# Performance work log

Measured on AMD Instinct MI355X. Metric: run time of the kernel, lower is better.

## Reference

```python
import jax, jax.numpy as jnp
import numpy as np

N = 100000
E = 3200000
H = 128
ED = 16
P = 6  # 2**(sample_hop+1)-2 with sample_hop=2


def setup_inputs() -> dict:
    key = jax.random.key(0)
    ks = jax.random.split(key, 8)
    q = jax.random.normal(ks[0], (N, H), jnp.float32)
    k = jax.random.normal(ks[1], (N, H), jnp.float32)
    v = jax.random.normal(ks[2], (N, H), jnp.float32)
    eigs = jax.random.normal(ks[3], (N, ED), jnp.float32)
    lambda0 = jnp.zeros((1,), jnp.float32)
    path_emb_w = jax.random.normal(ks[4], (P, 1), jnp.float32)
    indices = jax.random.randint(ks[5], (2, E), 0, N, dtype=jnp.int32)
    path_type = jax.random.randint(ks[6], (E,), 0, P, dtype=jnp.int32)
    return {"q": q, "k": k, "v": v, "eigs": eigs, "lambda0": lambda0,
            "path_emb_w": path_emb_w, "indices": indices, "path_type": path_type}


def _segment_softmax(vals, seg, num_segments):
    # numerically stable softmax over edges grouped by destination row `seg`
    m = jax.ops.segment_max(vals, seg, num_segments=num_segments)
    m = jnp.where(jnp.isfinite(m), m, 0.0)  # empty segments -> 0, harmless
    e = jnp.exp(vals - m[seg])
    d = jax.ops.segment_sum(e, seg, num_segments=num_segments)
    return e / d[seg]


def reference(q, k, v, eigs, lambda0, path_emb_w, indices, path_type):
    row, col = indices[0], indices[1]
    inv_sqrt_dim = 1.0 / jnp.sqrt(jnp.float32(H))
    # per-edge q.k score  [E]
    x = jnp.sum(q[row] * k[col], axis=-1) * inv_sqrt_dim
    # eig bias  [E]
    y = jnp.sum(eigs[row] * eigs[col], axis=-1)
    s0 = x + jnp.exp(lambda0[0]) * y
    # path bias  [E]
    s1 = path_emb_w[path_type, 0]
    a0 = _segment_softmax(s0, row, N)
    a1 = _segment_softmax(s1, row, N)
    s = 0.5 * (a0 + a1)  # stack+mean over the two score channels
    # sparse [N,N] @ v : scatter-add weighted value rows
    out = jax.ops.segment_sum(s[:, None] * v[col], row, num_segments=N)
    return out
```

## Files before the change

### kernel.cpp

```cpp
#include <hip/hip_runtime.h>
#include <math.h>

#define H 128
#define ED 16
#define COLBITS 17
#define COLMASK 0x1FFFF

__device__ __forceinline__ float wsum64(float v) {
#pragma unroll
    for (int o = 32; o > 0; o >>= 1) v += __shfl_xor(v, o, 64);
    return v;
}
__device__ __forceinline__ float wmax64(float v) {
#pragma unroll
    for (int o = 32; o > 0; o >>= 1) v = fmaxf(v, __shfl_xor(v, o, 64));
    return v;
}
__device__ __forceinline__ float bflo(unsigned u) { return __uint_as_float(u << 16); }
__device__ __forceinline__ float bfhi(unsigned u) { return __uint_as_float(u & 0xffff0000u); }
__device__ __forceinline__ unsigned short f2bf(float f) {
    unsigned u = __float_as_uint(f);
    return (unsigned short)((u + 0x7fff + ((u >> 16) & 1)) >> 16);
}

__global__ __launch_bounds__(256) void k_cast2(const float4* __restrict__ k,
                                               const float4* __restrict__ v,
                                               ushort4* __restrict__ kb,
                                               ushort4* __restrict__ vb, int n4) {
    int i = blockIdx.x * 256 + threadIdx.x;
    const float4* src;
    ushort4* dst;
    int j;
    if (i < n4) {
        src = k; dst = kb; j = i;
    } else if (i < 2 * n4) {
        src = v; dst = vb; j = i - n4;
    } else {
        return;
    }
    float4 f = src[j];
    ushort4 o;
    o.x = f2bf(f.x);
    o.y = f2bf(f.y);
    o.z = f2bf(f.z);
    o.w = f2bf(f.w);
    dst[j] = o;
}

__global__ __launch_bounds__(256) void k_count(const int* __restrict__ rows,
                                               int* __restrict__ bcnt, int E, int nb) {
    __shared__ int h[512];
    int t = threadIdx.x;
    h[t] = 0;
    h[t + 256] = 0;
    __syncthreads();
    int base = blockIdx.x * 4096;
#pragma unroll
    for (int j = 0; j < 4; j++) {
        int e = base + j * 1024 + t * 4;
        if (e + 3 < E) {
            int4 r = *(const int4*)(rows + e);
            atomicAdd(&h[r.x >> 8], 1);
            atomicAdd(&h[r.y >> 8], 1);
            atomicAdd(&h[r.z >> 8], 1);
            atomicAdd(&h[r.w >> 8], 1);
        } else {
#pragma unroll
            for (int q = 0; q < 4; q++) {
                int e2 = e + q;
                if (e2 < E) atomicAdd(&h[rows[e2] >> 8], 1);
            }
        }
    }
    __syncthreads();
    for (int i = t; i < nb; i += 256) {
        int c = h[i];
        if (c) atomicAdd(&bcnt[i], c);
    }
}

__global__ void k_scan_bb(const int* __restrict__ bcnt, int* __restrict__ bbase,
                          int* __restrict__ bcur, int* __restrict__ rowstart, int nb,
                          int N, int E) {
    __shared__ int tmp[512];
    int t = threadIdx.x;
    int v = (t < nb) ? bcnt[t] : 0;
    tmp[t] = v;
    __syncthreads();
#pragma unroll
    for (int o = 1; o < 512; o <<= 1) {
        int x = (t >= o) ? tmp[t - o] : 0;
        __syncthreads();
        if (t >= o) tmp[t] += x;
        __syncthreads();
    }
    if (t < nb) {
        int ex = tmp[t] - v;
        bbase[t] = ex;
        bcur[t] = ex;
    }
    if (t == 0) {
        bbase[nb] = E;
        rowstart[N] = E;
    }
}

__global__ __launch_bounds__(256) void k_bucket(const int* __restrict__ rows,
                                                const int* __restrict__ cols,
                                                const int* __restrict__ pts,
                                                int* __restrict__ bcur,
                                                int* __restrict__ stage, int E, int nb) {
    __shared__ int h[512];
    __shared__ int lbase[512];
    int t = threadIdx.x;
    h[t] = 0;
    h[t + 256] = 0;
    __syncthreads();
    int base = blockIdx.x * 4096;
    int pr[16];
    int br[16];
#pragma unroll
    for (int j = 0; j < 4; j++) {
        int e = base + j * 1024 + t * 4;
        if (e + 3 < E) {
            int4 r = *(const int4*)(rows + e);
            int4 c = *(const int4*)(cols + e);
            int4 p = *(const int4*)(pts + e);
            int k0 = atomicAdd(&h[r.x >> 8], 1);
            int k1 = atomicAdd(&h[r.y >> 8], 1);
            int k2 = atomicAdd(&h[r.z >> 8], 1);
            int k3 = atomicAdd(&h[r.w >> 8], 1);
            br[j * 4 + 0] = ((r.x >> 8) << 16) | k0;
            br[j * 4 + 1] = ((r.y >> 8) << 16) | k1;
            br[j * 4 + 2] = ((r.z >> 8) << 16) | k2;
            br[j * 4 + 3] = ((r.w >> 8) << 16) | k3;
            pr[j * 4 + 0] = ((r.x & 255) << 20) | (p.x << COLBITS) | c.x;
            pr[j * 4 + 1] = ((r.y & 255) << 20) | (p.y << COLBITS) | c.y;
            pr[j * 4 + 2] = ((r.z & 255) << 20) | (p.z << COLBITS) | c.z;
            pr[j * 4 + 3] = ((r.w & 255) << 20) | (p.w << COLBITS) | c.w;
        } else {
#pragma unroll
            for (int q = 0; q < 4; q++) {
                int e2 = e + q;
                if (e2 < E) {
                    int r = rows[e2], c = cols[e2], p = pts[e2];
                    int kk = atomicAdd(&h[r >> 8], 1);
                    br[j * 4 + q] = ((r >> 8) << 16) | kk;
                    pr[j * 4 + q] = ((r & 255) << 20) | (p << COLBITS) | c;
                } else {
                    br[j * 4 + q] = -1;
                }
            }
        }
    }
    __syncthreads();
    for (int i = t; i < nb; i += 256) {
        int c = h[i];
        lbase[i] = c ? atomicAdd(&bcur[i], c) : 0;
    }
    __syncthreads();
#pragma unroll
    for (int j = 0; j < 16; j++) {
        int brv = br[j];
        if (brv >= 0) {
            int bin = brv >> 16;
            stage[lbase[bin] + (brv & 0xFFFF)] = pr[j];
        }
    }
}

__global__ __launch_bounds__(256) void k_build(const int* __restrict__ bbase,
                                               const int* __restrict__ stage,
                                               int* __restrict__ csr,
                                               int* __restrict__ rowstart, int N) {
    __shared__ int h[256];
    __shared__ int sc[256];
    __shared__ int cur[256];
    int b = blockIdx.x;
    int t = threadIdx.x;
    int s = bbase[b];
    int n = bbase[b + 1] - s;
    h[t] = 0;
    __syncthreads();
    for (int i = t; i < n; i += 256) atomicAdd(&h[stage[s + i] >> 20], 1);
    __syncthreads();
    int val = h[t];
    sc[t] = val;
    __syncthreads();
#pragma unroll
    for (int o = 1; o < 256; o <<= 1) {
        int x = (t >= o) ? sc[t - o] : 0;
        __syncthreads();
        if (t >= o) sc[t] += x;
        __syncthreads();
    }
    int excl = sc[t] - val;
    int row = (b << 8) + t;
    if (row < N) rowstart[row] = s + excl;
    cur[t] = excl;
    __syncthreads();
    for (int i = t; i < n; i += 256) {
        int v = stage[s + i];
        int p = atomicAdd(&cur[v >> 20], 1);
        csr[s + p] = v & 0xFFFFF;
    }
}

__global__ __launch_bounds__(256) void k_attn(
    const float* __restrict__ q, const unsigned short* __restrict__ kb,
    const unsigned short* __restrict__ vb, const float* __restrict__ eigs,
    const float* __restrict__ lambda0, const float* __restrict__ pw,
    const int* __restrict__ rowstart, const int* __restrict__ csr,
    float* __restrict__ spill, float* __restrict__ out, int N) {
    const int lane = threadIdx.x & 63;
    const int g = lane >> 4;
    const int s16 = lane & 15;
    const int rowi = blockIdx.x * 4 + (threadIdx.x >> 6);
    if (rowi >= N) return;

    const float el0 = __expf(lambda0[0]);
    const float inv = 0.08838834764831845f;
    const int start = rowstart[rowi];
    const int deg = rowstart[rowi + 1] - start;

    const float4* q4 = (const float4*)q;
    const float4* e4 = (const float4*)eigs;

    if (deg == 0) {
        if (g == 0) {
            float4 z = make_float4(0.f, 0.f, 0.f, 0.f);
            ((float4*)out)[(size_t)rowi * 32 + s16 * 2] = z;
            ((float4*)out)[(size_t)rowi * 32 + s16 * 2 + 1] = z;
        }
        return;
    }

    if (deg <= 128) {
        float s00 = -INFINITY, s01 = -INFINITY, t10 = -INFINITY, t11 = -INFINITY;
        {
            int e0 = 4 * s16 + g;
            if (e0 < deg) t10 = pw[(csr[start + e0] >> COLBITS) & 7];
            int e1 = 64 + 4 * s16 + g;
            if (e1 < deg) t11 = pw[(csr[start + e1] >> COLBITS) & 7];
        }
        float4 qa = q4[(size_t)rowi * 32 + s16 * 2];
        float4 qb = q4[(size_t)rowi * 32 + s16 * 2 + 1];
        float4 ea = make_float4(0.f, 0.f, 0.f, 0.f);
        if (s16 < 4) ea = e4[(size_t)rowi * 4 + s16];

        const int niter = (deg + 3) >> 2;

#pragma unroll 8
        for (int i = 0; i < niter; i++) {
            int rel = 4 * i + g;
            float p = 0.f;
            if (rel < deg) {
                int cm = csr[start + rel] & COLMASK;
                uint4 kr = *(const uint4*)(kb + (size_t)cm * H + s16 * 8);
                p = (qa.x * bflo(kr.x) + qa.y * bfhi(kr.x) + qa.z * bflo(kr.y) +
                     qa.w * bfhi(kr.y) + qb.x * bflo(kr.z) + qb.y * bfhi(kr.z) +
                     qb.z * bflo(kr.w) + qb.w * bfhi(kr.w)) * inv;
                if (s16 < 4) {
                    float4 ev = e4[(size_t)cm * 4 + s16];
                    p += el0 * (ea.x * ev.x + ea.y * ev.y + ea.z * ev.z + ea.w * ev.w);
                }
            }
#pragma unroll
            for (int o = 1; o < 16; o <<= 1) p += __shfl_xor(p, o, 64);
            if (s16 == (i & 15) && rel < deg) {
                if (i < 16) s00 = p;
                else s01 = p;
            }
        }

        float m0 = wmax64(fmaxf(s00, s01));
        float m1 = wmax64(fmaxf(t10, t11));
        float p00 = __expf(s00 - m0), p01 = __expf(s01 - m0);
        float p10 = __expf(t10 - m1), p11 = __expf(t11 - m1);
        float d0 = wsum64(p00 + p01);
        float d1 = wsum64(p10 + p11);
        float r0 = (d0 > 0.f) ? 0.5f / d0 : 0.f;
        float r1 = (d1 > 0.f) ? 0.5f / d1 : 0.f;
        float w0 = p00 * r0 + p10 * r1;
        float w1 = p01 * r0 + p11 * r1;

        float4 acc_a = make_float4(0.f, 0.f, 0.f, 0.f);
        float4 acc_b = make_float4(0.f, 0.f, 0.f, 0.f);
#pragma unroll 8
        for (int i = 0; i < niter; i++) {
            int rel = 4 * i + g;
            int src = (g << 4) | (i & 15);
            float wj = __shfl((i < 16) ? w0 : w1, src, 64);
            if (rel < deg) {
                int cm = csr[start + rel] & COLMASK;
                uint4 vr = *(const uint4*)(vb + (size_t)cm * H + s16 * 8);
                acc_a.x = fmaf(wj, bflo(vr.x), acc_a.x);
                acc_a.y = fmaf(wj, bfhi(vr.x), acc_a.y);
                acc_a.z = fmaf(wj, bflo(vr.y), acc_a.z);
                acc_a.w = fmaf(wj, bfhi(vr.y), acc_a.w);
                acc_b.x = fmaf(wj, bflo(vr.z), acc_b.x);
                acc_b.y = fmaf(wj, bfhi(vr.z), acc_b.y);
                acc_b.z = fmaf(wj, bflo(vr.w), acc_b.z);
                acc_b.w = fmaf(wj, bfhi(vr.w), acc_b.w);
            }
        }
#pragma unroll
        for (int o = 16; o < 64; o <<= 1) {
            acc_a.x += __shfl_xor(acc_a.x, o, 64);
            acc_a.y += __shfl_xor(acc_a.y, o, 64);
            acc_a.z += __shfl_xor(acc_a.z, o, 64);
            acc_a.w += __shfl_xor(acc_a.w, o, 64);
            acc_b.x += __shfl_xor(acc_b.x, o, 64);
            acc_b.y += __shfl_xor(acc_b.y, o, 64);
            acc_b.z += __shfl_xor(acc_b.z, o, 64);
            acc_b.w += __shfl_xor(acc_b.w, o, 64);
        }
        if (g == 0) {
            ((float4*)out)[(size_t)rowi * 32 + s16 * 2] = acc_a;
            ((float4*)out)[(size_t)rowi * 32 + s16 * 2 + 1] = acc_b;
        }
        return;
    }

    const int end = start + deg;
    const float2* q2r = (const float2*)(q + (size_t)rowi * H);
    const float4* erow = (const float4*)(eigs + (size_t)rowi * ED);
    float m0 = -INFINITY, m1 = -INFINITY;
    for (int e0 = start; e0 < end; e0 += 64) {
        int e = e0 + lane;
        float s0f = -INFINITY, s1f = -INFINITY;
        if (e < end) {
            int x = csr[e];
            int cc = x & COLMASK;
            s1f = pw[(x >> COLBITS) & 7];
            const unsigned* kr = (const unsigned*)(kb + (size_t)cc * H);
            float xx = 0.f;
            for (int t = 0; t < H / 2; t++) {
                unsigned u = kr[t];
                float2 qv = q2r[t];
                xx += qv.x * bflo(u) + qv.y * bfhi(u);
            }
            const float4* crow = (const float4*)(eigs + (size_t)cc * ED);
            float yy = 0.f;
#pragma unroll
            for (int t = 0; t < ED / 4; t++) {
                float4 ev = erow[t], cv = crow[t];
                yy += ev.x * cv.x + ev.y * cv.y + ev.z * cv.z + ev.w * cv.w;
            }
            s0f = xx * inv + el0 * yy;
            spill[e] = s0f;
        }
        m0 = fmaxf(m0, s0f);
        m1 = fmaxf(m1, s1f);
    }
    m0 = wmax64(m0);
    m1 = wmax64(m1);
    float d0 = 0.f, d1 = 0.f;
    for (int e0 = start; e0 < end; e0 += 64) {
        int e = e0 + lane;
        if (e < end) {
            int x = csr[e];
            d0 += __expf(spill[e] - m0);
            d1 += __expf(pw[(x >> COLBITS) & 7] - m1);
        }
    }
    d0 = wsum64(d0);
    d1 = wsum64(d1);
    float r0 = (d0 > 0.f) ? 0.5f / d0 : 0.f;
    float r1 = (d1 > 0.f) ? 0.5f / d1 : 0.f;
    float2 acc2 = make_float2(0.f, 0.f);
    for (int e0 = start; e0 < end; e0 += 64) {
        int cnt2 = min(64, end - e0);
        int cc = 0;
        float wv = 0.f;
        if (lane < cnt2) {
            int e = e0 + lane;
            int x = csr[e];
            cc = x & COLMASK;
            wv = __expf(spill[e] - m0) * r0 + __expf(pw[(x >> COLBITS) & 7] - m1) * r1;
        }
        for (int j = 0; j < cnt2; j++) {
            float wj = __shfl(wv, j, 64);
            int cj = __shfl(cc, j, 64);
            unsigned u = ((const unsigned*)(vb))[(size_t)cj * (H / 2) + lane];
            acc2.x = fmaf(wj, bflo(u), acc2.x);
            acc2.y = fmaf(wj, bfhi(u), acc2.y);
        }
    }
    ((float2*)out)[(size_t)rowi * (H / 2) + lane] = acc2;
}

extern "C" void kernel_launch(void* const* d_in, const int* in_sizes, int n_in,
                              void* d_out, int out_size, void* d_ws, size_t ws_size,
                              hipStream_t stream) {
    const float* q = (const float*)d_in[0];
    const float* k = (const float*)d_in[1];
    const float* v = (const float*)d_in[2];
    const float* eigs = (const float*)d_in[3];
    const float* lambda0 = (const float*)d_in[4];
    const float* pw = (const float*)d_in[5];
    const int* indices = (const int*)d_in[6];
    const int* ptype = (const int*)d_in[7];
    float* out = (float*)d_out;

    int N = in_sizes[0] / H;
    int E = in_sizes[6] / 2;
    int nb = (N + 255) >> 8;

    char* ws = (char*)d_ws;
    int* bcnt = (int*)ws;
    int* bbase = bcnt + nb;
    int* bcur = bbase + (nb + 1);
    int* rowstart = bcur + nb;
    size_t off = ((size_t)(3 * nb + 1 + N + 1) * 4 + 15) & ~(size_t)15;
    int* stage = (int*)(ws + off);
    off += (size_t)E * 4;
    int* csr = (int*)(ws + off);
    off += (size_t)E * 4;
    unsigned short* kb = (unsigned short*)(ws + off);
    off += (size_t)N * H * 2;
    unsigned short* vb = (unsigned short*)(ws + off);

    hipMemsetAsync(bcnt, 0, (size_t)nb * sizeof(int), stream);

    int n4 = N * H / 4;
    int nbC = (2 * n4 + 255) / 256;
    k_cast2<<<nbC, 256, 0, stream>>>((const float4*)k, (const float4*)v, (ushort4*)kb,
                                     (ushort4*)vb, n4);

    int nbE = (E + 4095) / 4096;
    k_count<<<nbE, 256, 0, stream>>>(indices, bcnt, E, nb);
    k_scan_bb<<<1, 512, 0, stream>>>(bcnt, bbase, bcur, rowstart, nb, N, E);
    k_bucket<<<nbE, 256, 0, stream>>>(indices, indices + E, ptype, bcur, stage, E, nb);
    k_build<<<nb, 256, 0, stream>>>(bbase, stage, csr, rowstart, N);
    k_attn<<<(N + 3) / 4, 256, 0, stream>>>(q, kb, vb, eigs, lambda0, pw, rowstart,
                                            csr, (float*)stage, out, N);
}
```

Before: 660.4 us.

## Fuse cast and count kernels, batch gathers and preload CSR in attention

The bf16 cast kernel and the row-bucket count kernel are merged into one launch, with the block index choosing the role, to save a launch and let the two overlap. In the attention kernel's small-degree path, each row's CSR entries are loaded once into registers and passed around with shuffles instead of being re-read in every iteration. The K, eig and V gathers are batched eight at a time so more loads are in flight before they are used. Launch bounds now request 4 waves per SIMD, which caps register use, and the eight-wide gather batches raise register pressure and could cause spills.

```diff
diff --git a/kernel.cpp b/kernel.cpp
--- a/kernel.cpp
+++ b/kernel.cpp
@@ -23,38 +23,40 @@
     return (unsigned short)((u + 0x7fff + ((u >> 16) & 1)) >> 16);
 }
 
-__global__ __launch_bounds__(256) void k_cast2(const float4* __restrict__ k,
-                                               const float4* __restrict__ v,
-                                               ushort4* __restrict__ kb,
-                                               ushort4* __restrict__ vb, int n4) {
-    int i = blockIdx.x * 256 + threadIdx.x;
-    const float4* src;
-    ushort4* dst;
-    int j;
-    if (i < n4) {
-        src = k; dst = kb; j = i;
-    } else if (i < 2 * n4) {
-        src = v; dst = vb; j = i - n4;
-    } else {
-        return;
-    }
-    float4 f = src[j];
-    ushort4 o;
-    o.x = f2bf(f.x);
-    o.y = f2bf(f.y);
-    o.z = f2bf(f.z);
-    o.w = f2bf(f.w);
-    dst[j] = o;
-}
-
-__global__ __launch_bounds__(256) void k_count(const int* __restrict__ rows,
-                                               int* __restrict__ bcnt, int E, int nb) {
+__global__ __launch_bounds__(256) void k_pre(const float4* __restrict__ k,
+                                             const float4* __restrict__ v,
+                                             ushort4* __restrict__ kb,
+                                             ushort4* __restrict__ vb, int n4,
+                                             const int* __restrict__ rows,
+                                             int* __restrict__ bcnt, int E, int nb,
+                                             int nbC) {
     __shared__ int h[512];
     int t = threadIdx.x;
+    if (blockIdx.x < nbC) {
+        int i = blockIdx.x * 256 + t;
+        const float4* src;
+        ushort4* dst;
+        int j;
+        if (i < n4) {
+            src = k; dst = kb; j = i;
+        } else if (i < 2 * n4) {
+            src = v; dst = vb; j = i - n4;
+        } else {
+            return;
+        }
+        float4 f = src[j];
+        ushort4 o;
+        o.x = f2bf(f.x);
+        o.y = f2bf(f.y);
+        o.z = f2bf(f.z);
+        o.w = f2bf(f.w);
+        dst[j] = o;
+        return;
+    }
     h[t] = 0;
     h[t + 256] = 0;
     __syncthreads();
-    int base = blockIdx.x * 4096;
+    int base = (blockIdx.x - nbC) * 4096;
 #pragma unroll
     for (int j = 0; j < 4; j++) {
         int e = base + j * 1024 + t * 4;
@@ -206,7 +208,7 @@
     }
 }
 
-__global__ __launch_bounds__(256) void k_attn(
+__global__ __launch_bounds__(256, 4) void k_attn(
     const float* __restrict__ q, const unsigned short* __restrict__ kb,
     const unsigned short* __restrict__ vb, const float* __restrict__ eigs,
     const float* __restrict__ lambda0, const float* __restrict__ pw,
@@ -236,12 +238,17 @@
     }
 
     if (deg <= 128) {
+        int c0 = 0, c1 = 0;
+        if (lane < deg) c0 = csr[start + lane];
+        if (64 + lane < deg) c1 = csr[start + 64 + lane];
+
         float s00 = -INFINITY, s01 = -INFINITY, t10 = -INFINITY, t11 = -INFINITY;
         {
             int e0 = 4 * s16 + g;
-            if (e0 < deg) t10 = pw[(csr[start + e0] >> COLBITS) & 7];
-            int e1 = 64 + 4 * s16 + g;
-            if (e1 < deg) t11 = pw[(csr[start + e1] >> COLBITS) & 7];
+            int cw0 = __shfl(c0, e0, 64);
+            int cw1 = __shfl(c1, e0, 64);
+            if (e0 < deg) t10 = pw[(cw0 >> COLBITS) & 7];
+            if (64 + e0 < deg) t11 = pw[(cw1 >> COLBITS) & 7];
         }
         float4 qa = q4[(size_t)rowi * 32 + s16 * 2];
         float4 qb = q4[(size_t)rowi * 32 + s16 * 2 + 1];
@@ -250,26 +257,43 @@
 
         const int niter = (deg + 3) >> 2;
 
-#pragma unroll 8
-        for (int i = 0; i < niter; i++) {
-            int rel = 4 * i + g;
-            float p = 0.f;
-            if (rel < deg) {
-                int cm = csr[start + rel] & COLMASK;
-                uint4 kr = *(const uint4*)(kb + (size_t)cm * H + s16 * 8);
-                p = (qa.x * bflo(kr.x) + qa.y * bfhi(kr.x) + qa.z * bflo(kr.y) +
-                     qa.w * bfhi(kr.y) + qb.x * bflo(kr.z) + qb.y * bfhi(kr.z) +
-                     qb.z * bflo(kr.w) + qb.w * bfhi(kr.w)) * inv;
-                if (s16 < 4) {
-                    float4 ev = e4[(size_t)cm * 4 + s16];
-                    p += el0 * (ea.x * ev.x + ea.y * ev.y + ea.z * ev.z + ea.w * ev.w);
+        for (int ib = 0; ib < niter; ib += 8) {
+            uint4 kr[8];
+            float4 er[8];
+            int cm[8];
+            bool vld[8];
+#pragma unroll
+            for (int u = 0; u < 8; u++) {
+                int i = ib + u;
+                int rel = 4 * i + g;
+                vld[u] = (rel < deg);
+                int cw = __shfl((i < 16) ? c0 : c1, rel & 63, 64);
+                cm[u] = cw & COLMASK;
+                if (vld[u]) kr[u] = *(const uint4*)(kb + (size_t)cm[u] * H + s16 * 8);
+            }
+#pragma unroll
+            for (int u = 0; u < 8; u++) {
+                if (vld[u] && s16 < 4) er[u] = e4[(size_t)cm[u] * 4 + s16];
+            }
+#pragma unroll
+            for (int u = 0; u < 8; u++) {
+                int i = ib + u;
+                float p = 0.f;
+                if (vld[u]) {
+                    p = (qa.x * bflo(kr[u].x) + qa.y * bfhi(kr[u].x) +
+                         qa.z * bflo(kr[u].y) + qa.w * bfhi(kr[u].y) +
+                         qb.x * bflo(kr[u].z) + qb.y * bfhi(kr[u].z) +
+                         qb.z * bflo(kr[u].w) + qb.w * bfhi(kr[u].w)) * inv;
+                    if (s16 < 4)
+                        p += el0 * (ea.x * er[u].x + ea.y * er[u].y + ea.z * er[u].z +
+                                    ea.w * er[u].w);
                 }
-            }
-#pragma unroll
-            for (int o = 1; o < 16; o <<= 1) p += __shfl_xor(p, o, 64);
-            if (s16 == (i & 15) && rel < deg) {
-                if (i < 16) s00 = p;
-                else s01 = p;
+#pragma unroll
+                for (int o = 1; o < 16; o <<= 1) p += __shfl_xor(p, o, 64);
+                if (s16 == (i & 15) && vld[u]) {
+                    if (i < 16) s00 = p;
+                    else s01 = p;
+                }
             }
         }
 
@@ -286,22 +310,33 @@
 
         float4 acc_a = make_float4(0.f, 0.f, 0.f, 0.f);
         float4 acc_b = make_float4(0.f, 0.f, 0.f, 0.f);
-#pragma unroll 8
-        for (int i = 0; i < niter; i++) {
-            int rel = 4 * i + g;
-            int src = (g << 4) | (i & 15);
-            float wj = __shfl((i < 16) ? w0 : w1, src, 64);
-            if (rel < deg) {
-                int cm = csr[start + rel] & COLMASK;
-                uint4 vr = *(const uint4*)(vb + (size_t)cm * H + s16 * 8);
-                acc_a.x = fmaf(wj, bflo(vr.x), acc_a.x);
-                acc_a.y = fmaf(wj, bfhi(vr.x), acc_a.y);
-                acc_a.z = fmaf(wj, bflo(vr.y), acc_a.z);
-                acc_a.w = fmaf(wj, bfhi(vr.y), acc_a.w);
-                acc_b.x = fmaf(wj, bflo(vr.z), acc_b.x);
-                acc_b.y = fmaf(wj, bfhi(vr.z), acc_b.y);
-                acc_b.z = fmaf(wj, bflo(vr.w), acc_b.z);
-                acc_b.w = fmaf(wj, bfhi(vr.w), acc_b.w);
+        for (int ib = 0; ib < niter; ib += 8) {
+            uint4 vr[8];
+            bool vld[8];
+#pragma unroll
+            for (int u = 0; u < 8; u++) {
+                int i = ib + u;
+                int rel = 4 * i + g;
+                vld[u] = (rel < deg);
+                int cw = __shfl((i < 16) ? c0 : c1, rel & 63, 64);
+                if (vld[u])
+                    vr[u] = *(const uint4*)(vb + (size_t)(cw & COLMASK) * H + s16 * 8);
+            }
+#pragma unroll
+            for (int u = 0; u < 8; u++) {
+                int i = ib + u;
+                int src = (g << 4) | (i & 15);
+                float wj = __shfl((i < 16) ? w0 : w1, src, 64);
+                if (vld[u]) {
+                    acc_a.x = fmaf(wj, bflo(vr[u].x), acc_a.x);
+                    acc_a.y = fmaf(wj, bfhi(vr[u].x), acc_a.y);
+                    acc_a.z = fmaf(wj, bflo(vr[u].y), acc_a.z);
+                    acc_a.w = fmaf(wj, bfhi(vr[u].y), acc_a.w);
+                    acc_b.x = fmaf(wj, bflo(vr[u].z), acc_b.x);
+                    acc_b.y = fmaf(wj, bfhi(vr[u].z), acc_b.y);
+                    acc_b.z = fmaf(wj, bflo(vr[u].w), acc_b.z);
+                    acc_b.w = fmaf(wj, bfhi(vr[u].w), acc_b.w);
+                }
             }
         }
 #pragma unroll
@@ -425,11 +460,10 @@
 
     int n4 = N * H / 4;
     int nbC = (2 * n4 + 255) / 256;
-    k_cast2<<<nbC, 256, 0, stream>>>((const float4*)k, (const float4*)v, (ushort4*)kb,
-                                     (ushort4*)vb, n4);
-
     int nbE = (E + 4095) / 4096;
-    k_count<<<nbE, 256, 0, stream>>>(indices, bcnt, E, nb);
+    k_pre<<<nbC + nbE, 256, 0, stream>>>((const float4*)k, (const float4*)v,
+                                         (ushort4*)kb, (ushort4*)vb, n4, indices, bcnt,
+                                         E, nb, nbC);
     k_scan_bb<<<1, 512, 0, stream>>>(bcnt, bbase, bcur, rowstart, nb, N, E);
     k_bucket<<<nbE, 256, 0, stream>>>(indices, indices + E, ptype, bcur, stage, E, nb);
     k_build<<<nb, 256, 0, stream>>>(bbase, stage, csr, rowstart, N);
```

New measurement: 679.8 us. +2.9%, slower.

## Fuse softmax and value aggregation into a single pass; merge cast and count kernels

Applied to the files above, without the earlier changes.

For rows with up to 128 edges, the attention kernel now reads K and V together in one loop. It accumulates exp-weighted value sums and denominators for both score channels, then normalises once at the end. This replaces the old two-pass scheme (scores, then a second gather of V) and drops the max subtraction, which risks overflow for large scores. Separately, the bf16 cast and the edge-count histogram are merged into one launch. The CSR build kernel now uses 1024 threads per block.

```diff
diff --git a/kernel.cpp b/kernel.cpp
--- a/kernel.cpp
+++ b/kernel.cpp
@@ -23,38 +23,40 @@
     return (unsigned short)((u + 0x7fff + ((u >> 16) & 1)) >> 16);
 }
 
-__global__ __launch_bounds__(256) void k_cast2(const float4* __restrict__ k,
-                                               const float4* __restrict__ v,
-                                               ushort4* __restrict__ kb,
-                                               ushort4* __restrict__ vb, int n4) {
-    int i = blockIdx.x * 256 + threadIdx.x;
-    const float4* src;
-    ushort4* dst;
-    int j;
-    if (i < n4) {
-        src = k; dst = kb; j = i;
-    } else if (i < 2 * n4) {
-        src = v; dst = vb; j = i - n4;
-    } else {
-        return;
-    }
-    float4 f = src[j];
-    ushort4 o;
-    o.x = f2bf(f.x);
-    o.y = f2bf(f.y);
-    o.z = f2bf(f.z);
-    o.w = f2bf(f.w);
-    dst[j] = o;
-}
-
-__global__ __launch_bounds__(256) void k_count(const int* __restrict__ rows,
-                                               int* __restrict__ bcnt, int E, int nb) {
+__global__ __launch_bounds__(256) void k_pre(const float4* __restrict__ k,
+                                             const float4* __restrict__ v,
+                                             ushort4* __restrict__ kb,
+                                             ushort4* __restrict__ vb, int n4,
+                                             const int* __restrict__ rows,
+                                             int* __restrict__ bcnt, int E, int nb,
+                                             int nbC) {
     __shared__ int h[512];
     int t = threadIdx.x;
+    if (blockIdx.x < nbC) {
+        int i = blockIdx.x * 256 + t;
+        const float4* src;
+        ushort4* dst;
+        int j;
+        if (i < n4) {
+            src = k; dst = kb; j = i;
+        } else if (i < 2 * n4) {
+            src = v; dst = vb; j = i - n4;
+        } else {
+            return;
+        }
+        float4 f = src[j];
+        ushort4 o;
+        o.x = f2bf(f.x);
+        o.y = f2bf(f.y);
+        o.z = f2bf(f.z);
+        o.w = f2bf(f.w);
+        dst[j] = o;
+        return;
+    }
     h[t] = 0;
     h[t + 256] = 0;
     __syncthreads();
-    int base = blockIdx.x * 4096;
+    int base = (blockIdx.x - nbC) * 4096;
 #pragma unroll
     for (int j = 0; j < 4; j++) {
         int e = base + j * 1024 + t * 4;
@@ -169,10 +171,10 @@
     }
 }
 
-__global__ __launch_bounds__(256) void k_build(const int* __restrict__ bbase,
-                                               const int* __restrict__ stage,
-                                               int* __restrict__ csr,
-                                               int* __restrict__ rowstart, int N) {
+__global__ __launch_bounds__(1024) void k_build(const int* __restrict__ bbase,
+                                                const int* __restrict__ stage,
+                                                int* __restrict__ csr,
+                                                int* __restrict__ rowstart, int N) {
     __shared__ int h[256];
     __shared__ int sc[256];
     __shared__ int cur[256];
@@ -180,26 +182,28 @@
     int t = threadIdx.x;
     int s = bbase[b];
     int n = bbase[b + 1] - s;
-    h[t] = 0;
-    __syncthreads();
-    for (int i = t; i < n; i += 256) atomicAdd(&h[stage[s + i] >> 20], 1);
-    __syncthreads();
-    int val = h[t];
-    sc[t] = val;
+    if (t < 256) h[t] = 0;
+    __syncthreads();
+    for (int i = t; i < n; i += 1024) atomicAdd(&h[stage[s + i] >> 20], 1);
+    __syncthreads();
+    int val = (t < 256) ? h[t] : 0;
+    if (t < 256) sc[t] = val;
     __syncthreads();
 #pragma unroll
     for (int o = 1; o < 256; o <<= 1) {
-        int x = (t >= o) ? sc[t - o] : 0;
+        int x = (t >= o && t < 256) ? sc[t - o] : 0;
         __syncthreads();
-        if (t >= o) sc[t] += x;
+        if (t >= o && t < 256) sc[t] += x;
         __syncthreads();
     }
-    int excl = sc[t] - val;
-    int row = (b << 8) + t;
-    if (row < N) rowstart[row] = s + excl;
-    cur[t] = excl;
-    __syncthreads();
-    for (int i = t; i < n; i += 256) {
+    if (t < 256) {
+        int excl = sc[t] - val;
+        int row = (b << 8) + t;
+        if (row < N) rowstart[row] = s + excl;
+        cur[t] = excl;
+    }
+    __syncthreads();
+    for (int i = t; i < n; i += 1024) {
         int v = stage[s + i];
         int p = atomicAdd(&cur[v >> 20], 1);
         csr[s + p] = v & 0xFFFFF;
@@ -236,88 +240,92 @@
     }
 
     if (deg <= 128) {
-        float s00 = -INFINITY, s01 = -INFINITY, t10 = -INFINITY, t11 = -INFINITY;
-        {
-            int e0 = 4 * s16 + g;
-            if (e0 < deg) t10 = pw[(csr[start + e0] >> COLBITS) & 7];
-            int e1 = 64 + 4 * s16 + g;
-            if (e1 < deg) t11 = pw[(csr[start + e1] >> COLBITS) & 7];
-        }
         float4 qa = q4[(size_t)rowi * 32 + s16 * 2];
         float4 qb = q4[(size_t)rowi * 32 + s16 * 2 + 1];
         float4 ea = make_float4(0.f, 0.f, 0.f, 0.f);
         if (s16 < 4) ea = e4[(size_t)rowi * 4 + s16];
 
+        float4 a0a = make_float4(0.f, 0.f, 0.f, 0.f);
+        float4 a0b = make_float4(0.f, 0.f, 0.f, 0.f);
+        float4 a1a = make_float4(0.f, 0.f, 0.f, 0.f);
+        float4 a1b = make_float4(0.f, 0.f, 0.f, 0.f);
+        float d0 = 0.f, d1 = 0.f;
+
         const int niter = (deg + 3) >> 2;
-
-#pragma unroll 8
+#pragma unroll 4
         for (int i = 0; i < niter; i++) {
             int rel = 4 * i + g;
+            bool val = rel < deg;
             float p = 0.f;
-            if (rel < deg) {
-                int cm = csr[start + rel] & COLMASK;
-                uint4 kr = *(const uint4*)(kb + (size_t)cm * H + s16 * 8);
+            float f1 = 0.f;
+            uint4 kr, vr;
+            if (val) {
+                int cw = csr[start + rel];
+                int cm = cw & COLMASK;
+                f1 = __expf(pw[(cw >> COLBITS) & 7]);
+                kr = *(const uint4*)(kb + (size_t)cm * H + s16 * 8);
+                vr = *(const uint4*)(vb + (size_t)cm * H + s16 * 8);
                 p = (qa.x * bflo(kr.x) + qa.y * bfhi(kr.x) + qa.z * bflo(kr.y) +
                      qa.w * bfhi(kr.y) + qb.x * bflo(kr.z) + qb.y * bfhi(kr.z) +
                      qb.z * bflo(kr.w) + qb.w * bfhi(kr.w)) * inv;
                 if (s16 < 4) {
-                    float4 ev = e4[(size_t)cm * 4 + s16];
+                    float4 ev = e4[(size_t)(cw & COLMASK) * 4 + s16];
                     p += el0 * (ea.x * ev.x + ea.y * ev.y + ea.z * ev.z + ea.w * ev.w);
                 }
             }
 #pragma unroll
             for (int o = 1; o < 16; o <<= 1) p += __shfl_xor(p, o, 64);
-            if (s16 == (i & 15) && rel < deg) {
-                if (i < 16) s00 = p;
-                else s01 = p;
-            }
-        }
-
-        float m0 = wmax64(fmaxf(s00, s01));
-        float m1 = wmax64(fmaxf(t10, t11));
-        float p00 = __expf(s00 - m0), p01 = __expf(s01 - m0);
-        float p10 = __expf(t10 - m1), p11 = __expf(t11 - m1);
-        float d0 = wsum64(p00 + p01);
-        float d1 = wsum64(p10 + p11);
-        float r0 = (d0 > 0.f) ? 0.5f / d0 : 0.f;
-        float r1 = (d1 > 0.f) ? 0.5f / d1 : 0.f;
-        float w0 = p00 * r0 + p10 * r1;
-        float w1 = p01 * r0 + p11 * r1;
-
-        float4 acc_a = make_float4(0.f, 0.f, 0.f, 0.f);
-        float4 acc_b = make_float4(0.f, 0.f, 0.f, 0.f);
-#pragma unroll 8
-        for (int i = 0; i < niter; i++) {
-            int rel = 4 * i + g;
-            int src = (g << 4) | (i & 15);
-            float wj = __shfl((i < 16) ? w0 : w1, src, 64);
-            if (rel < deg) {
-                int cm = csr[start + rel] & COLMASK;
-                uint4 vr = *(const uint4*)(vb + (size_t)cm * H + s16 * 8);
-                acc_a.x = fmaf(wj, bflo(vr.x), acc_a.x);
-                acc_a.y = fmaf(wj, bfhi(vr.x), acc_a.y);
-                acc_a.z = fmaf(wj, bflo(vr.y), acc_a.z);
-                acc_a.w = fmaf(wj, bfhi(vr.y), acc_a.w);
-                acc_b.x = fmaf(wj, bflo(vr.z), acc_b.x);
-                acc_b.y = fmaf(wj, bfhi(vr.z), acc_b.y);
-                acc_b.z = fmaf(wj, bflo(vr.w), acc_b.z);
-                acc_b.w = fmaf(wj, bfhi(vr.w), acc_b.w);
-            }
-        }
+            if (val) {
+                float f0 = __expf(p);
+                d0 += f0;
+                d1 += f1;
+                a0a.x = fmaf(f0, bflo(vr.x), a0a.x);
+                a0a.y = fmaf(f0, bfhi(vr.x), a0a.y);
+                a0a.z = fmaf(f0, bflo(vr.y), a0a.z);
+                a0a.w = fmaf(f0, bfhi(vr.y), a0a.w);
+                a0b.x = fmaf(f0, bflo(vr.z), a0b.x);
+                a0b.y = fmaf(f0, bfhi(vr.z), a0b.y);
+                a0b.z = fmaf(f0, bflo(vr.w), a0b.z);
+                a0b.w = fmaf(f0, bfhi(vr.w), a0b.w);
+                a1a.x = fmaf(f1, bflo(vr.x), a1a.x);
+                a1a.y = fmaf(f1, bfhi(vr.x), a1a.y);
+                a1a.z = fmaf(f1, bflo(vr.y), a1a.z);
+                a1a.w = fmaf(f1, bfhi(vr.y), a1a.w);
+                a1b.x = fmaf(f1, bflo(vr.z), a1b.x);
+                a1b.y = fmaf(f1, bfhi(vr.z), a1b.y);
+                a1b.z = fmaf(f1, bflo(vr.w), a1b.z);
+                a1b.w = fmaf(f1, bfhi(vr.w), a1b.w);
+            }
+        }
+
+        float d0t = wsum64(d0) * 0.0625f;
+        float d1t = wsum64(d1) * 0.0625f;
+        float r0 = (d0t > 0.f) ? 0.5f / d0t : 0.f;
+        float r1 = (d1t > 0.f) ? 0.5f / d1t : 0.f;
+
+        float4 oa, ob;
+        oa.x = r0 * a0a.x + r1 * a1a.x;
+        oa.y = r0 * a0a.y + r1 * a1a.y;
+        oa.z = r0 * a0a.z + r1 * a1a.z;
+        oa.w = r0 * a0a.w + r1 * a1a.w;
+        ob.x = r0 * a0b.x + r1 * a1b.x;
+        ob.y = r0 * a0b.y + r1 * a1b.y;
+        ob.z = r0 * a0b.z + r1 * a1b.z;
+        ob.w = r0 * a0b.w + r1 * a1b.w;
 #pragma unroll
         for (int o = 16; o < 64; o <<= 1) {
-            acc_a.x += __shfl_xor(acc_a.x, o, 64);
-            acc_a.y += __shfl_xor(acc_a.y, o, 64);
-            acc_a.z += __shfl_xor(acc_a.z, o, 64);
-            acc_a.w += __shfl_xor(acc_a.w, o, 64);
-            acc_b.x += __shfl_xor(acc_b.x, o, 64);
-            acc_b.y += __shfl_xor(acc_b.y, o, 64);
-            acc_b.z += __shfl_xor(acc_b.z, o, 64);
-            acc_b.w += __shfl_xor(acc_b.w, o, 64);
+            oa.x += __shfl_xor(oa.x, o, 64);
+            oa.y += __shfl_xor(oa.y, o, 64);
+            oa.z += __shfl_xor(oa.z, o, 64);
+            oa.w += __shfl_xor(oa.w, o, 64);
+            ob.x += __shfl_xor(ob.x, o, 64);
+            ob.y += __shfl_xor(ob.y, o, 64);
+            ob.z += __shfl_xor(ob.z, o, 64);
+            ob.w += __shfl_xor(ob.w, o, 64);
         }
         if (g == 0) {
-            ((float4*)out)[(size_t)rowi * 32 + s16 * 2] = acc_a;
-            ((float4*)out)[(size_t)rowi * 32 + s16 * 2 + 1] = acc_b;
+            ((float4*)out)[(size_t)rowi * 32 + s16 * 2] = oa;
+            ((float4*)out)[(size_t)rowi * 32 + s16 * 2 + 1] = ob;
         }
         return;
     }
@@ -425,14 +433,13 @@
 
     int n4 = N * H / 4;
     int nbC = (2 * n4 + 255) / 256;
-    k_cast2<<<nbC, 256, 0, stream>>>((const float4*)k, (const float4*)v, (ushort4*)kb,
-                                     (ushort4*)vb, n4);
-
     int nbE = (E + 4095) / 4096;
-    k_count<<<nbE, 256, 0, stream>>>(indices, bcnt, E, nb);
+    k_pre<<<nbC + nbE, 256, 0, stream>>>((const float4*)k, (const float4*)v,
+                                         (ushort4*)kb, (ushort4*)vb, n4, indices, bcnt,
+                                         E, nb, nbC);
     k_scan_bb<<<1, 512, 0, stream>>>(bcnt, bbase, bcur, rowstart, nb, N, E);
     k_bucket<<<nbE, 256, 0, stream>>>(indices, indices + E, ptype, bcur, stage, E, nb);
-    k_build<<<nb, 256, 0, stream>>>(bbase, stage, csr, rowstart, N);
+    k_build<<<nb, 1024, 0, stream>>>(bbase, stage, csr, rowstart, N);
     k_attn<<<(N + 3) / 4, 256, 0, stream>>>(q, kb, vb, eigs, lambda0, pw, rowstart,
                                             csr, (float*)stage, out, N);
 }
```

Result: faster. 641.9 us (-2.8%).
